# Performance work log

Hardware: AMD Instinct MI355X
Metric: run time of the kernel (lower is better)

Reference implementation:

```python
import jax, jax.numpy as jnp
import numpy as np

B, L, E = 16, 192, 128
T = 25  # hardcoded self.season_len in the original module


def setup_inputs() -> dict:
    key = jax.random.key(0)
    kx, kw, kb = jax.random.split(key, 3)
    x = jax.random.normal(kx, (B, L, E), dtype=jnp.float32)
    # nn.Linear(1, 2): weight [2,1], bias [2]
    W = jax.random.normal(kw, (2, 1), dtype=jnp.float32)
    b = jax.random.normal(kb, (2,), dtype=jnp.float32)
    return {"x": x, "W": W, "b": b}


def reference(x, W, b):
    # x: [B, L, E]. Faithful to the torch forward:
    #   for i <= T: append x[:, i:i+1, :]                 -> [B,1,E]
    #   for i >  T: append sum(stack(x_i, x_{i-T}) * softmax(Linear(x[...,None])), -1)
    #               which broadcasts to a full [B,L,E] block (softmax over the
    #               2-way Linear output is identical for every i, so compute once).
    Bb, Ll, Ee = x.shape
    logits = x[..., None] * W[:, 0] + b                # [B,L,E,2]
    s = jax.nn.softmax(logits, axis=-1)                # [B,L,E,2]
    idx = jnp.arange(T + 1, Ll)                        # i = 26 .. L-1  (M = L-26)
    xi = x[:, idx, :]                                  # [B,M,E]  x[:, i, :]
    xp = x[:, idx - T, :]                              # [B,M,E]  x[:, i-T, :]
    # blocks[b,i,l,e] = xi[b,i,e]*s[b,l,e,0] + xp[b,i,e]*s[b,l,e,1]
    blocks = (xi[:, :, None, :] * s[:, None, :, :, 0]
              + xp[:, :, None, :] * s[:, None, :, :, 1])  # [B,M,L,E]
    blocks = blocks.reshape(Bb, -1, Ee)                # [B, M*L, E]
    # loop order: i=0..T first (identity rows), then the big blocks in order
    return jnp.concatenate([x[:, :T + 1, :], blocks], axis=1)  # [B, T+1 + M*L, E]
```

## Files before the change

### kernel.cpp

```cpp
#include <hip/hip_runtime.h>

constexpr int Bn = 16;
constexpr int L  = 192;
constexpr int E  = 128;
constexpr int T  = 25;
constexpr int NI = L - T - 1;
constexpr int ROWS_OUT = (T + 1) + NI * L;
constexpr int E4 = E / 4;

__global__ __launch_bounds__(256) void seasonality_kernel(
    const float* __restrict__ x,
    const float* __restrict__ W,
    const float* __restrict__ bv,
    float* __restrict__ out)
{
    const int blk = blockIdx.x;
    const int t = threadIdx.x;

    if (blk < Bn * L) {
        const int b = blk / L;
        const int l = blk % L;
        const int e4 = t & (E4 - 1);
        const int i0 = t >> 5;

        const float4* __restrict__ xb = (const float4*)(x + (size_t)b * L * E);
        float4* __restrict__ ob = (float4*)(out + (size_t)b * ROWS_OUT * E);

        const float dw = W[1] - W[0];
        const float db = bv[1] - bv[0];
        const float4 xv = xb[(size_t)l * E4 + e4];
        float4 s0;
        s0.x = 1.0f / (1.0f + expf(xv.x * dw + db));
        s0.y = 1.0f / (1.0f + expf(xv.y * dw + db));
        s0.z = 1.0f / (1.0f + expf(xv.z * dw + db));
        s0.w = 1.0f / (1.0f + expf(xv.w * dw + db));

        for (int i = i0; i < NI; i += 8) {
            const float4 xi = xb[(size_t)(T + 1 + i) * E4 + e4];
            const float4 xp = xb[(size_t)(1 + i) * E4 + e4];
            float4 o;
            o.x = xp.x + (xi.x - xp.x) * s0.x;
            o.y = xp.y + (xi.y - xp.y) * s0.y;
            o.z = xp.z + (xi.z - xp.z) * s0.z;
            o.w = xp.w + (xi.w - xp.w) * s0.w;
            ob[(size_t)(T + 1 + i * L + l) * E4 + e4] = o;
        }
    } else {
        const int gid = (blk - Bn * L) * 256 + t;
        constexpr int per_b = (T + 1) * E4;
        constexpr int total = Bn * per_b;
        if (gid < total) {
            const int b = gid / per_b;
            const int r = gid % per_b;
            const float4* __restrict__ xb = (const float4*)(x + (size_t)b * L * E);
            float4* __restrict__ ob = (float4*)(out + (size_t)b * ROWS_OUT * E);
            ob[r] = xb[r];
        }
    }
}

extern "C" void kernel_launch(void* const* d_in, const int* in_sizes, int n_in,
                              void* d_out, int out_size, void* d_ws, size_t ws_size,
                              hipStream_t stream) {
    const float* x  = (const float*)d_in[0];
    const float* W  = (const float*)d_in[1];
    const float* bv = (const float*)d_in[2];
    float* out = (float*)d_out;

    constexpr int prefix_f4 = Bn * (T + 1) * E4;
    constexpr int prefix_blocks = (prefix_f4 + 255) / 256;
    const int grid = Bn * L + prefix_blocks;

    seasonality_kernel<<<grid, 256, 0, stream>>>(x, W, bv, out);
}
```

Measured before the change: 293.3 us.

## Precompute sigmoid plane in workspace and restructure blocks kernel per output row-block

Splits the work into a sigmoid precompute kernel that writes the softmax weight plane to the workspace, then a blocks kernel where each workgroup owns one (batch, i) output block and streams the contiguous L*E plane with coalesced reads and nontemporal stores. The output is roughly 100M floats (about 400 MB), so the kernel is bound by write bandwidth. The new mapping gives each block contiguous output writes instead of row-strided scatter across i. It also uses fast exp/rcp intrinsics and keeps an inline fallback when no workspace is available. The cost is a second launch and extra reads of the sigmoid plane per block, which should mostly hit cache, plus slightly lower precision in the sigmoid.

```diff
diff --git a/kernel.cpp b/kernel.cpp
--- a/kernel.cpp
+++ b/kernel.cpp
@@ -7,8 +7,78 @@
 constexpr int NI = L - T - 1;
 constexpr int ROWS_OUT = (T + 1) + NI * L;
 constexpr int E4 = E / 4;
+constexpr int S_ELEMS = Bn * L * E;
+constexpr int PLANE_F4 = L * E4;
 
-__global__ __launch_bounds__(256) void seasonality_kernel(
+typedef float f4 __attribute__((ext_vector_type(4)));
+
+__global__ __launch_bounds__(256) void sigmoid_kernel(
+    const float* __restrict__ x,
+    const float* __restrict__ W,
+    const float* __restrict__ bv,
+    float* __restrict__ s)
+{
+    const int g = blockIdx.x * 256 + threadIdx.x;
+    if (g >= S_ELEMS / 4) return;
+    const float dw = W[1] - W[0];
+    const float db = bv[1] - bv[0];
+    const f4 xv = ((const f4*)x)[g];
+    f4 o;
+    o.x = __builtin_amdgcn_rcpf(1.0f + __expf(fmaf(xv.x, dw, db)));
+    o.y = __builtin_amdgcn_rcpf(1.0f + __expf(fmaf(xv.y, dw, db)));
+    o.z = __builtin_amdgcn_rcpf(1.0f + __expf(fmaf(xv.z, dw, db)));
+    o.w = __builtin_amdgcn_rcpf(1.0f + __expf(fmaf(xv.w, dw, db)));
+    ((f4*)s)[g] = o;
+}
+
+__global__ __launch_bounds__(256) void blocks_kernel(
+    const float* __restrict__ x,
+    const float* __restrict__ s,
+    float* __restrict__ out)
+{
+    const int blk = blockIdx.x;
+    const int t = threadIdx.x;
+
+    if (blk < Bn * NI) {
+        const int b = blk / NI;
+        const int i = blk % NI;
+        const int e4 = t & (E4 - 1);
+
+        const f4* __restrict__ xrow_i = (const f4*)(x + ((size_t)(b * L + T + 1 + i)) * E);
+        const f4* __restrict__ xrow_p = (const f4*)(x + ((size_t)(b * L + 1 + i)) * E);
+        const f4 xp4 = xrow_p[e4];
+        const f4 xi4 = xrow_i[e4];
+        const f4 d4 = xi4 - xp4;
+
+        const f4* __restrict__ sp = (const f4*)(s) + (size_t)b * PLANE_F4;
+        f4* __restrict__ ob = (f4*)(out) + ((size_t)b * ROWS_OUT + (T + 1) + (size_t)i * L) * E4;
+
+        #pragma unroll 4
+        for (int k = 0; k < PLANE_F4 / 256; ++k) {
+            const int j = k * 256 + t;
+            const f4 s4 = sp[j];
+            f4 o;
+            o.x = fmaf(d4.x, s4.x, xp4.x);
+            o.y = fmaf(d4.y, s4.y, xp4.y);
+            o.z = fmaf(d4.z, s4.z, xp4.z);
+            o.w = fmaf(d4.w, s4.w, xp4.w);
+            __builtin_nontemporal_store(o, &ob[j]);
+        }
+    } else {
+        const int gid = (blk - Bn * NI) * 256 + t;
+        constexpr int per_b = (T + 1) * E4;
+        constexpr int total = Bn * per_b;
+        if (gid < total) {
+            const int b = gid / per_b;
+            const int r = gid % per_b;
+            const f4* __restrict__ xb = (const f4*)(x + (size_t)b * L * E);
+            f4* __restrict__ ob = (f4*)(out + (size_t)b * ROWS_OUT * E);
+            __builtin_nontemporal_store(xb[r], &ob[r]);
+        }
+    }
+}
+
+__global__ __launch_bounds__(256) void blocks_kernel_inline(
     const float* __restrict__ x,
     const float* __restrict__ W,
     const float* __restrict__ bv,
@@ -16,45 +86,43 @@
 {
     const int blk = blockIdx.x;
     const int t = threadIdx.x;
+    const float dw = W[1] - W[0];
+    const float db = bv[1] - bv[0];
 
-    if (blk < Bn * L) {
-        const int b = blk / L;
-        const int l = blk % L;
+    if (blk < Bn * NI) {
+        const int b = blk / NI;
+        const int i = blk % NI;
         const int e4 = t & (E4 - 1);
-        const int i0 = t >> 5;
 
-        const float4* __restrict__ xb = (const float4*)(x + (size_t)b * L * E);
-        float4* __restrict__ ob = (float4*)(out + (size_t)b * ROWS_OUT * E);
+        const f4* __restrict__ xrow_i = (const f4*)(x + ((size_t)(b * L + T + 1 + i)) * E);
+        const f4* __restrict__ xrow_p = (const f4*)(x + ((size_t)(b * L + 1 + i)) * E);
+        const f4 xp4 = xrow_p[e4];
+        const f4 xi4 = xrow_i[e4];
+        const f4 d4 = xi4 - xp4;
 
-        const float dw = W[1] - W[0];
-        const float db = bv[1] - bv[0];
-        const float4 xv = xb[(size_t)l * E4 + e4];
-        float4 s0;
-        s0.x = 1.0f / (1.0f + expf(xv.x * dw + db));
-        s0.y = 1.0f / (1.0f + expf(xv.y * dw + db));
-        s0.z = 1.0f / (1.0f + expf(xv.z * dw + db));
-        s0.w = 1.0f / (1.0f + expf(xv.w * dw + db));
+        const f4* __restrict__ xp_plane = (const f4*)(x) + (size_t)b * PLANE_F4;
+        f4* __restrict__ ob = (f4*)(out) + ((size_t)b * ROWS_OUT + (T + 1) + (size_t)i * L) * E4;
 
-        for (int i = i0; i < NI; i += 8) {
-            const float4 xi = xb[(size_t)(T + 1 + i) * E4 + e4];
-            const float4 xp = xb[(size_t)(1 + i) * E4 + e4];
-            float4 o;
-            o.x = xp.x + (xi.x - xp.x) * s0.x;
-            o.y = xp.y + (xi.y - xp.y) * s0.y;
-            o.z = xp.z + (xi.z - xp.z) * s0.z;
-            o.w = xp.w + (xi.w - xp.w) * s0.w;
-            ob[(size_t)(T + 1 + i * L + l) * E4 + e4] = o;
+        for (int k = 0; k < PLANE_F4 / 256; ++k) {
+            const int j = k * 256 + t;
+            const f4 xv = xp_plane[j];
+            f4 o;
+            o.x = fmaf(d4.x, __builtin_amdgcn_rcpf(1.0f + __expf(fmaf(xv.x, dw, db))), xp4.x);
+            o.y = fmaf(d4.y, __builtin_amdgcn_rcpf(1.0f + __expf(fmaf(xv.y, dw, db))), xp4.y);
+            o.z = fmaf(d4.z, __builtin_amdgcn_rcpf(1.0f + __expf(fmaf(xv.z, dw, db))), xp4.z);
+            o.w = fmaf(d4.w, __builtin_amdgcn_rcpf(1.0f + __expf(fmaf(xv.w, dw, db))), xp4.w);
+            __builtin_nontemporal_store(o, &ob[j]);
         }
     } else {
-        const int gid = (blk - Bn * L) * 256 + t;
+        const int gid = (blk - Bn * NI) * 256 + t;
         constexpr int per_b = (T + 1) * E4;
         constexpr int total = Bn * per_b;
         if (gid < total) {
             const int b = gid / per_b;
             const int r = gid % per_b;
-            const float4* __restrict__ xb = (const float4*)(x + (size_t)b * L * E);
-            float4* __restrict__ ob = (float4*)(out + (size_t)b * ROWS_OUT * E);
-            ob[r] = xb[r];
+            const f4* __restrict__ xb = (const f4*)(x + (size_t)b * L * E);
+            f4* __restrict__ ob = (f4*)(out + (size_t)b * ROWS_OUT * E);
+            __builtin_nontemporal_store(xb[r], &ob[r]);
         }
     }
 }
@@ -69,7 +137,13 @@
 
     constexpr int prefix_f4 = Bn * (T + 1) * E4;
     constexpr int prefix_blocks = (prefix_f4 + 255) / 256;
-    const int grid = Bn * L + prefix_blocks;
+    const int grid2 = Bn * NI + prefix_blocks;
 
-    seasonality_kernel<<<grid, 256, 0, stream>>>(x, W, bv, out);
+    if (ws_size >= (size_t)S_ELEMS * sizeof(float)) {
+        float* s = (float*)d_ws;
+        sigmoid_kernel<<<(S_ELEMS / 4 + 255) / 256, 256, 0, stream>>>(x, W, bv, s);
+        blocks_kernel<<<grid2, 256, 0, stream>>>(x, s, out);
+    } else {
+        blocks_kernel_inline<<<grid2, 256, 0, stream>>>(x, W, bv, out);
+    }
 }
```

Result: faster. 267.6 us (-8.8%).
